# Performance work log

Measured on AMD Instinct MI355X. Metric: run time of the kernel, lower is better.

Reference implementation:

```python
import jax, jax.numpy as jnp
import numpy as np

H_DIM = 64
GRID = 8
NS = 2.0  # neighborhood_size


def _pool_seq(hidden, pos):
    # hidden: (P, H_DIM) hidden states of peds in one scene; pos: (P, 2) end positions
    P = hidden.shape[0]
    g2 = GRID * GRID
    tl_x = pos[:, 0] - NS / 2
    tl_y = pos[:, 1] + NS / 2
    br_x = pos[:, 0] + NS / 2
    br_y = pos[:, 1] - NS / 2
    # pair (i, j): grid of ped i (rows), position of ped j (cols)
    ox = pos[None, :, 0]
    oy = pos[None, :, 1]
    cell_x = jnp.floor((ox - tl_x[:, None]) / NS * GRID)
    cell_y = jnp.floor((tl_y[:, None] - oy) / NS * GRID)
    grid_pos = (cell_x + cell_y * GRID).astype(jnp.int32)
    # out-of-bound if outside neighborhood box OR i == j (diagonal forced out)
    oob = ((ox >= br_x[:, None]) | (ox <= tl_x[:, None])
           | (oy >= tl_y[:, None]) | (oy <= br_y[:, None])
           | jnp.eye(P, dtype=bool))
    idx = grid_pos + 1 + (jnp.arange(P, dtype=jnp.int32) * g2)[:, None]
    idx = jnp.where(oob, 0, idx)  # slot 0 is the trash bin (dropped below)
    src = jnp.broadcast_to(hidden[None], (P, P, H_DIM)).reshape(P * P, H_DIM)
    buf = jnp.zeros((P * g2 + 1, H_DIM), hidden.dtype)
    buf = buf.at[idx.reshape(-1)].add(src)
    return buf[1:].reshape(P, g2 * H_DIM)


def reference(h_states, seq_start_end, end_pos, rel_pos, W, b):
    B = end_pos.shape[0]
    S = seq_start_end.shape[0]
    P = B // S  # equal-length scenes -> static reshape
    hidden = h_states.reshape(-1, H_DIM).reshape(S, P, H_DIM)
    pos = end_pos.reshape(S, P, 2)
    pooled = jax.vmap(_pool_seq)(hidden, pos).reshape(B, GRID * GRID * H_DIM)
    # make_mlp([4096, 1024], relu, batch_norm=False): Linear -> ReLU
    return jax.nn.relu(pooled @ W + b)


def setup_inputs():
    key = jax.random.key(0)
    k0, k1, k2, k3 = jax.random.split(key, 4)
    S, P = 64, 64
    B = S * P
    bottleneck = 1024
    feat = GRID * GRID * H_DIM  # 4096
    h_states = jax.random.normal(k0, (1, B, H_DIM), jnp.float32)
    starts = jnp.arange(S, dtype=jnp.int32) * P
    seq_start_end = jnp.stack([starts, starts + P], axis=1)
    end_pos = jax.random.normal(k1, (B, 2), jnp.float32)
    rel_pos = jax.random.normal(k2, (B, 2), jnp.float32)
    W = jax.random.normal(k3, (feat, bottleneck), jnp.float32) * 0.02
    b = jnp.zeros((bottleneck,), jnp.float32)
    return {"h_states": h_states, "seq_start_end": seq_start_end,
            "end_pos": end_pos, "rel_pos": rel_pos, "W": W, "b": b}
```

## Files before the change

### kernel.cpp

```cpp
#include <hip/hip_runtime.h>


#define BM 128
#define BN 64
#define BK 128

typedef short short8 __attribute__((ext_vector_type(8)));
typedef short short4v __attribute__((ext_vector_type(4)));
typedef float floatx16 __attribute__((ext_vector_type(16)));

__device__ inline short f2bf(float x) {
    union { float f; unsigned u; } v; v.f = x;
    unsigned r = v.u + 0x7fffu + ((v.u >> 16) & 1u);
    return (short)(r >> 16);
}

__device__ inline void gload_lds16(const void* g, void* l) {
    __builtin_amdgcn_global_load_lds(
        (const __attribute__((address_space(1))) void*)g,
        (__attribute__((address_space(3))) void*)l,
        16, 0, 0);
}

__global__ __launch_bounds__(256) void prep_kernel(
    const float* __restrict__ h,
    const float* __restrict__ pos,
    short* __restrict__ pooled,
    const float* __restrict__ W,
    short* __restrict__ Wt,
    int K, int N, int poolBlocks)
{
    __shared__ __align__(16) unsigned char sh[18944];
    const int tid = threadIdx.x;

    if ((int)blockIdx.x < poolBlocks) {
        float* hs = (float*)sh;
        float* px = (float*)(sh + 16384);
        float* py = (float*)(sh + 16640);
        unsigned long long* wmask = (unsigned long long*)(sh + 16896);

        const int lane = tid & 63;
        const int w    = tid >> 6;
        const int s    = blockIdx.x >> 4;
        const int grp  = blockIdx.x & 15;
        const size_t base = (size_t)s * 64;

        const float4* hv  = (const float4*)(h + base * 64);
        float4*       hsv = (float4*)hs;
        #pragma unroll
        for (int c = 0; c < 4; ++c) hsv[tid + c * 256] = hv[tid + c * 256];
        if (tid < 64) {
            float2 p = ((const float2*)pos)[base + tid];
            px[tid] = p.x; py[tid] = p.y;
        }
        wmask[w * 64 + lane] = 0ull;
        __syncthreads();

        const int i = grp * 4 + w;
        const float tlx = px[i] - 1.0f;
        const float tly = py[i] + 1.0f;
        const float brx = px[i] + 1.0f;
        const float bry = py[i] - 1.0f;

        {
            const int j = lane;
            const float ox = px[j], oy = py[j];
            if (ox < brx && ox > tlx && oy < tly && oy > bry && j != i) {
                int cx = (int)floorf((ox - tlx) * 4.0f);
                int cy = (int)floorf((tly - oy) * 4.0f);
                atomicOr(&wmask[w * 64 + cx + cy * 8], 1ull << j);
            }
        }

        const int d = lane;
        const size_t orow = (base + i) * 4096;
        for (int c = 0; c < 64; ++c) {
            unsigned long long m = wmask[w * 64 + c];
            float a0 = 0.f, a1 = 0.f;
            while (m) {
                int j0 = __builtin_ctzll(m); m &= m - 1;
                if (m) {
                    int j1 = __builtin_ctzll(m); m &= m - 1;
                    a1 += hs[j1 * 64 + d];
                }
                a0 += hs[j0 * 64 + d];
            }
            pooled[orow + c * 64 + d] = f2bf(a0 + a1);
        }
    } else {
        float* t = (float*)sh;
        const int bid = blockIdx.x - poolBlocks;
        const int k0 = (bid & 63) * 64;
        const int n0 = (bid >> 6) * 64;

        const int r  = tid >> 4;
        const int cq = (tid & 15) * 4;
        #pragma unroll
        for (int i2 = 0; i2 < 4; ++i2) {
            const int row = r + i2 * 16;
            float4 v = *(const float4*)&W[(size_t)(k0 + row) * N + n0 + cq];
            t[row * 65 + cq + 0] = v.x; t[row * 65 + cq + 1] = v.y;
            t[row * 65 + cq + 2] = v.z; t[row * 65 + cq + 3] = v.w;
        }
        __syncthreads();
        const int nl = tid >> 4;
        const int kq = (tid & 15) * 4;
        #pragma unroll
        for (int i2 = 0; i2 < 4; ++i2) {
            const int n = nl + i2 * 16;
            short4v o;
            o.x = f2bf(t[(kq + 0) * 65 + n]); o.y = f2bf(t[(kq + 1) * 65 + n]);
            o.z = f2bf(t[(kq + 2) * 65 + n]); o.w = f2bf(t[(kq + 3) * 65 + n]);
            *(short4v*)&Wt[(size_t)(n0 + n) * K + k0 + kq] = o;
        }
    }
}

__global__ __launch_bounds__(256) void gemm_bias_relu(
    const short* __restrict__ A,
    const short* __restrict__ Bt,
    const float* __restrict__ bias,
    float* __restrict__ out,
    int M, int N, int K)
{
    __shared__ __align__(16) short As[BM * BK];
    __shared__ __align__(16) short Bs[BN * BK];

    const int tid  = threadIdx.x;
    const int lane = tid & 63;
    const int wave = tid >> 6;
    const int wr = wave >> 1;
    const int wc = wave & 1;
    const int nl = lane & 31;
    const int hl = lane >> 5;
    const int ml = lane & 15;

    const int b  = blockIdx.x;
    const int ib = b >> 3;
    const int m0 = ((b & 7) * 4 + (ib >> 4)) * BM;
    const int n0 = (ib & 15) * BN;

    const int r4   = lane >> 4;
    const int slot = lane & 15;

    const short* ag[8];
    const short* bg[4];
    #pragma unroll
    for (int c = 0; c < 8; ++c) {
        const int gi = c * 4 + wave;
        const int rl = gi * 4 + r4;
        ag[c] = A + (size_t)(m0 + rl) * K + (slot ^ (rl & 15)) * 8;
    }
    #pragma unroll
    for (int c = 0; c < 4; ++c) {
        const int gi = c * 4 + wave;
        const int rl = gi * 4 + r4;
        bg[c] = Bt + (size_t)(n0 + rl) * K + (slot ^ (rl & 15)) * 8;
    }

    floatx16 acc[2];
    #pragma unroll
    for (int mt = 0; mt < 2; ++mt)
        #pragma unroll
        for (int r = 0; r < 16; ++r) acc[mt][r] = 0.f;

    for (int kb = 0; kb < K; kb += BK) {
        if (kb) __syncthreads();
        #pragma unroll
        for (int c = 0; c < 8; ++c) {
            gload_lds16(ag[c], &As[(c * 4 + wave) * 512]);
            ag[c] += BK;
        }
        #pragma unroll
        for (int c = 0; c < 4; ++c) {
            gload_lds16(bg[c], &Bs[(c * 4 + wave) * 512]);
            bg[c] += BK;
        }
        __syncthreads();

        #pragma unroll
        for (int t = 0; t < 8; ++t) {
            const int g  = 2 * t + hl;
            short8 a0 = *(const short8*)&As[(wr * 64 +      nl) * BK + ((g ^ ml) * 8)];
            short8 a1 = *(const short8*)&As[(wr * 64 + 32 + nl) * BK + ((g ^ ml) * 8)];
            short8 bfr = *(const short8*)&Bs[(wc * 32 +     nl) * BK + ((g ^ ml) * 8)];
            acc[0] = __builtin_amdgcn_mfma_f32_32x32x16_bf16(a0, bfr, acc[0], 0, 0, 0);
            acc[1] = __builtin_amdgcn_mfma_f32_32x32x16_bf16(a1, bfr, acc[1], 0, 0, 0);
        }
    }

    const int gn = n0 + wc * 32 + nl;
    const float bv = bias[gn];
    #pragma unroll
    for (int mt = 0; mt < 2; ++mt) {
        #pragma unroll
        for (int r = 0; r < 16; ++r) {
            const int row32 = (r & 3) + 8 * (r >> 2) + 4 * hl;
            const int gm = m0 + wr * 64 + mt * 32 + row32;
            float v = acc[mt][r] + bv;
            out[(size_t)gm * N + gn] = v > 0.f ? v : 0.f;
        }
    }
}

extern "C" void kernel_launch(void* const* d_in, const int* in_sizes, int n_in,
                              void* d_out, int out_size, void* d_ws, size_t ws_size,
                              hipStream_t stream) {
    const float* h    = (const float*)d_in[0];
    const float* pos  = (const float*)d_in[2];
    const float* W    = (const float*)d_in[4];
    const float* bias = (const float*)d_in[5];

    const int B = in_sizes[0] / 64;
    const int N = in_sizes[5];
    const int K = 64 * 64;

    short* pooled = (short*)d_ws;
    short* Wt     = pooled + (size_t)B * K;
    float* out    = (float*)d_out;

    const int poolBlocks = B / 4;
    const int castBlocks = (K / 64) * (N / 64);
    prep_kernel<<<poolBlocks + castBlocks, 256, 0, stream>>>(
        h, pos, pooled, W, Wt, K, N, poolBlocks);
    gemm_bias_relu<<<(B / BM) * (N / BN), 256, 0, stream>>>(
        pooled, Wt, bias, out, B, N, K);
}
```

Before: 133.3 us.

## Double-buffer GEMM LDS tiles and enlarge N tile to 128

The bf16 GEMM now uses a 128x128 output tile with BK=64, so each wave computes a 2x2 set of 32x32 MFMA tiles and reuses each loaded fragment more often. LDS is double-buffered: the next K slice is fetched with global_load_lds while the current one is consumed, leaving one barrier per iteration. This is meant to hide global-load latency and raise arithmetic intensity. The cost is half as many blocks (256 workgroups), more accumulator registers, and a changed XOR swizzle for the 64-wide rows.

```diff
diff --git a/kernel.cpp b/kernel.cpp
--- a/kernel.cpp
+++ b/kernel.cpp
@@ -2,8 +2,8 @@
 
 
 #define BM 128
-#define BN 64
-#define BK 128
+#define BN 128
+#define BK 64
 
 typedef short short8 __attribute__((ext_vector_type(8)));
 typedef short short4v __attribute__((ext_vector_type(4)));
@@ -123,8 +123,7 @@
     float* __restrict__ out,
     int M, int N, int K)
 {
-    __shared__ __align__(16) short As[BM * BK];
-    __shared__ __align__(16) short Bs[BN * BK];
+    __shared__ __align__(16) short smem[2][2][BM * BK];
 
     const int tid  = threadIdx.x;
     const int lane = tid & 63;
@@ -133,72 +132,81 @@
     const int wc = wave & 1;
     const int nl = lane & 31;
     const int hl = lane >> 5;
-    const int ml = lane & 15;
+    const int k7 = nl & 7;
 
     const int b  = blockIdx.x;
     const int ib = b >> 3;
-    const int m0 = ((b & 7) * 4 + (ib >> 4)) * BM;
-    const int n0 = (ib & 15) * BN;
-
-    const int r4   = lane >> 4;
-    const int slot = lane & 15;
-
-    const short* ag[8];
+    const int m0 = ((b & 7) * 4 + (ib >> 3)) * BM;
+    const int n0 = (ib & 7) * BN;
+
+    const int r8    = lane >> 3;
+    const int slot3 = lane & 7;
+
+    const short* ag[4];
     const short* bg[4];
     #pragma unroll
-    for (int c = 0; c < 8; ++c) {
-        const int gi = c * 4 + wave;
-        const int rl = gi * 4 + r4;
-        ag[c] = A + (size_t)(m0 + rl) * K + (slot ^ (rl & 15)) * 8;
-    }
-    #pragma unroll
     for (int c = 0; c < 4; ++c) {
-        const int gi = c * 4 + wave;
-        const int rl = gi * 4 + r4;
-        bg[c] = Bt + (size_t)(n0 + rl) * K + (slot ^ (rl & 15)) * 8;
-    }
-
-    floatx16 acc[2];
-    #pragma unroll
-    for (int mt = 0; mt < 2; ++mt)
-        #pragma unroll
-        for (int r = 0; r < 16; ++r) acc[mt][r] = 0.f;
+        const int g  = c * 4 + wave;
+        const int rl = g * 8 + r8;
+        ag[c] = A  + (size_t)(m0 + rl) * K + (slot3 ^ (rl & 7)) * 8;
+        bg[c] = Bt + (size_t)(n0 + rl) * K + (slot3 ^ (rl & 7)) * 8;
+    }
+
+    floatx16 acc[2][2];
+    #pragma unroll
+    for (int i = 0; i < 2; ++i)
+        #pragma unroll
+        for (int j = 0; j < 2; ++j)
+            #pragma unroll
+            for (int r = 0; r < 16; ++r) acc[i][j][r] = 0.f;
+
+    #pragma unroll
+    for (int c = 0; c < 4; ++c) {
+        gload_lds16(ag[c], &smem[0][0][(c * 4 + wave) * 512]);
+        gload_lds16(bg[c], &smem[0][1][(c * 4 + wave) * 512]);
+        ag[c] += BK; bg[c] += BK;
+    }
+    __syncthreads();
 
     for (int kb = 0; kb < K; kb += BK) {
-        if (kb) __syncthreads();
-        #pragma unroll
-        for (int c = 0; c < 8; ++c) {
-            gload_lds16(ag[c], &As[(c * 4 + wave) * 512]);
-            ag[c] += BK;
-        }
-        #pragma unroll
-        for (int c = 0; c < 4; ++c) {
-            gload_lds16(bg[c], &Bs[(c * 4 + wave) * 512]);
-            bg[c] += BK;
+        const int bu = (kb >> 6) & 1;
+        if (kb + BK < K) {
+            #pragma unroll
+            for (int c = 0; c < 4; ++c) {
+                gload_lds16(ag[c], &smem[bu ^ 1][0][(c * 4 + wave) * 512]);
+                gload_lds16(bg[c], &smem[bu ^ 1][1][(c * 4 + wave) * 512]);
+                ag[c] += BK; bg[c] += BK;
+            }
+        }
+        #pragma unroll
+        for (int t = 0; t < 4; ++t) {
+            const int g = 2 * t + hl;
+            const int go = (g ^ k7) * 8;
+            short8 a0 = *(const short8*)&smem[bu][0][(wr * 64 +      nl) * BK + go];
+            short8 a1 = *(const short8*)&smem[bu][0][(wr * 64 + 32 + nl) * BK + go];
+            short8 b0 = *(const short8*)&smem[bu][1][(wc * 64 +      nl) * BK + go];
+            short8 b1 = *(const short8*)&smem[bu][1][(wc * 64 + 32 + nl) * BK + go];
+            acc[0][0] = __builtin_amdgcn_mfma_f32_32x32x16_bf16(a0, b0, acc[0][0], 0, 0, 0);
+            acc[0][1] = __builtin_amdgcn_mfma_f32_32x32x16_bf16(a0, b1, acc[0][1], 0, 0, 0);
+            acc[1][0] = __builtin_amdgcn_mfma_f32_32x32x16_bf16(a1, b0, acc[1][0], 0, 0, 0);
+            acc[1][1] = __builtin_amdgcn_mfma_f32_32x32x16_bf16(a1, b1, acc[1][1], 0, 0, 0);
         }
         __syncthreads();
-
-        #pragma unroll
-        for (int t = 0; t < 8; ++t) {
-            const int g  = 2 * t + hl;
-            short8 a0 = *(const short8*)&As[(wr * 64 +      nl) * BK + ((g ^ ml) * 8)];
-            short8 a1 = *(const short8*)&As[(wr * 64 + 32 + nl) * BK + ((g ^ ml) * 8)];
-            short8 bfr = *(const short8*)&Bs[(wc * 32 +     nl) * BK + ((g ^ ml) * 8)];
-            acc[0] = __builtin_amdgcn_mfma_f32_32x32x16_bf16(a0, bfr, acc[0], 0, 0, 0);
-            acc[1] = __builtin_amdgcn_mfma_f32_32x32x16_bf16(a1, bfr, acc[1], 0, 0, 0);
-        }
-    }
-
-    const int gn = n0 + wc * 32 + nl;
-    const float bv = bias[gn];
-    #pragma unroll
-    for (int mt = 0; mt < 2; ++mt) {
-        #pragma unroll
-        for (int r = 0; r < 16; ++r) {
-            const int row32 = (r & 3) + 8 * (r >> 2) + 4 * hl;
-            const int gm = m0 + wr * 64 + mt * 32 + row32;
-            float v = acc[mt][r] + bv;
-            out[(size_t)gm * N + gn] = v > 0.f ? v : 0.f;
+    }
+
+    #pragma unroll
+    for (int jt = 0; jt < 2; ++jt) {
+        const int gn = n0 + wc * 64 + jt * 32 + nl;
+        const float bv = bias[gn];
+        #pragma unroll
+        for (int mt = 0; mt < 2; ++mt) {
+            #pragma unroll
+            for (int r = 0; r < 16; ++r) {
+                const int row32 = (r & 3) + 8 * (r >> 2) + 4 * hl;
+                const int gm = m0 + wr * 64 + mt * 32 + row32;
+                float v = acc[mt][jt][r] + bv;
+                out[(size_t)gm * N + gn] = v > 0.f ? v : 0.f;
+            }
         }
     }
 }
```

Measured after the change: 135.6 us. Within noise of the previous version (+1.8%).

## Write pooled A in MFMA fragment layout and load A directly from global

Applied to the files above, without the earlier changes.

The pooling stage now writes the bf16 pooled matrix in a pre-swizzled layout that matches the 32x32x16 MFMA operand fragment. The GEMM then reads A fragments straight from global memory into registers and drops the A staging through LDS. This removes LDS traffic, LDS capacity and global_load_lds work for A, which could allow higher occupancy. In exchange, A loads are no longer shared across the two column waves, so global/L2 reads of A double, and the pooling stores become scattered with a stride.

```diff
diff --git a/kernel.cpp b/kernel.cpp
--- a/kernel.cpp
+++ b/kernel.cpp
@@ -25,7 +25,7 @@
 __global__ __launch_bounds__(256) void prep_kernel(
     const float* __restrict__ h,
     const float* __restrict__ pos,
-    short* __restrict__ pooled,
+    short* __restrict__ Afr,
     const float* __restrict__ W,
     short* __restrict__ Wt,
     int K, int N, int poolBlocks)
@@ -73,19 +73,24 @@
         }
 
         const int d = lane;
-        const size_t orow = (base + i) * 4096;
+        const int m = (int)base + i;
+        const size_t pbase = (size_t)(m >> 5) * 131072
+                           + (size_t)(d >> 4) * 512
+                           + (size_t)((d >> 3) & 1) * 256
+                           + (size_t)(m & 31) * 8
+                           + (size_t)(d & 7);
         for (int c = 0; c < 64; ++c) {
-            unsigned long long m = wmask[w * 64 + c];
+            unsigned long long mk = wmask[w * 64 + c];
             float a0 = 0.f, a1 = 0.f;
-            while (m) {
-                int j0 = __builtin_ctzll(m); m &= m - 1;
-                if (m) {
-                    int j1 = __builtin_ctzll(m); m &= m - 1;
+            while (mk) {
+                int j0 = __builtin_ctzll(mk); mk &= mk - 1;
+                if (mk) {
+                    int j1 = __builtin_ctzll(mk); mk &= mk - 1;
                     a1 += hs[j1 * 64 + d];
                 }
                 a0 += hs[j0 * 64 + d];
             }
-            pooled[orow + c * 64 + d] = f2bf(a0 + a1);
+            Afr[pbase + (size_t)c * 2048] = f2bf(a0 + a1);
         }
     } else {
         float* t = (float*)sh;
@@ -117,13 +122,12 @@
 }
 
 __global__ __launch_bounds__(256) void gemm_bias_relu(
-    const short* __restrict__ A,
+    const short* __restrict__ Afr,
     const short* __restrict__ Bt,
     const float* __restrict__ bias,
     float* __restrict__ out,
     int M, int N, int K)
 {
-    __shared__ __align__(16) short As[BM * BK];
     __shared__ __align__(16) short Bs[BN * BK];
 
     const int tid  = threadIdx.x;
@@ -137,20 +141,12 @@
 
     const int b  = blockIdx.x;
     const int ib = b >> 3;
-    const int m0 = ((b & 7) * 4 + (ib >> 4)) * BM;
+    const int mb = (b & 7) * 4 + (ib >> 4);
     const int n0 = (ib & 15) * BN;
 
     const int r4   = lane >> 4;
     const int slot = lane & 15;
-
-    const short* ag[8];
     const short* bg[4];
-    #pragma unroll
-    for (int c = 0; c < 8; ++c) {
-        const int gi = c * 4 + wave;
-        const int rl = gi * 4 + r4;
-        ag[c] = A + (size_t)(m0 + rl) * K + (slot ^ (rl & 15)) * 8;
-    }
     #pragma unroll
     for (int c = 0; c < 4; ++c) {
         const int gi = c * 4 + wave;
@@ -158,6 +154,9 @@
         bg[c] = Bt + (size_t)(n0 + rl) * K + (slot ^ (rl & 15)) * 8;
     }
 
+    const short* a0p = Afr + ((size_t)(mb * 4 + wr * 2) * 256) * 512 + (size_t)lane * 8;
+    const short* a1p = a0p + 131072;
+
     floatx16 acc[2];
     #pragma unroll
     for (int mt = 0; mt < 2; ++mt)
@@ -167,23 +166,20 @@
     for (int kb = 0; kb < K; kb += BK) {
         if (kb) __syncthreads();
         #pragma unroll
-        for (int c = 0; c < 8; ++c) {
-            gload_lds16(ag[c], &As[(c * 4 + wave) * 512]);
-            ag[c] += BK;
-        }
-        #pragma unroll
         for (int c = 0; c < 4; ++c) {
             gload_lds16(bg[c], &Bs[(c * 4 + wave) * 512]);
             bg[c] += BK;
         }
         __syncthreads();
 
+        const int tbase = kb >> 4;
         #pragma unroll
         for (int t = 0; t < 8; ++t) {
-            const int g  = 2 * t + hl;
-            short8 a0 = *(const short8*)&As[(wr * 64 +      nl) * BK + ((g ^ ml) * 8)];
-            short8 a1 = *(const short8*)&As[(wr * 64 + 32 + nl) * BK + ((g ^ ml) * 8)];
-            short8 bfr = *(const short8*)&Bs[(wc * 32 +     nl) * BK + ((g ^ ml) * 8)];
+            const int koff = (tbase + t) * 512;
+            short8 a0 = *(const short8*)(a0p + koff);
+            short8 a1 = *(const short8*)(a1p + koff);
+            const int g = 2 * t + hl;
+            short8 bfr = *(const short8*)&Bs[(wc * 32 + nl) * BK + ((g ^ ml) * 8)];
             acc[0] = __builtin_amdgcn_mfma_f32_32x32x16_bf16(a0, bfr, acc[0], 0, 0, 0);
             acc[1] = __builtin_amdgcn_mfma_f32_32x32x16_bf16(a1, bfr, acc[1], 0, 0, 0);
         }
@@ -196,7 +192,7 @@
         #pragma unroll
         for (int r = 0; r < 16; ++r) {
             const int row32 = (r & 3) + 8 * (r >> 2) + 4 * hl;
-            const int gm = m0 + wr * 64 + mt * 32 + row32;
+            const int gm = mb * BM + wr * 64 + mt * 32 + row32;
             float v = acc[mt][r] + bv;
             out[(size_t)gm * N + gn] = v > 0.f ? v : 0.f;
         }
@@ -215,14 +211,14 @@
     const int N = in_sizes[5];
     const int K = 64 * 64;
 
-    short* pooled = (short*)d_ws;
-    short* Wt     = pooled + (size_t)B * K;
-    float* out    = (float*)d_out;
+    short* Afr = (short*)d_ws;
+    short* Wt  = Afr + (size_t)B * K;
+    float* out = (float*)d_out;
 
     const int poolBlocks = B / 4;
     const int castBlocks = (K / 64) * (N / 64);
     prep_kernel<<<poolBlocks + castBlocks, 256, 0, stream>>>(
-        h, pos, pooled, W, Wt, K, N, poolBlocks);
+        h, pos, Afr, W, Wt, K, N, poolBlocks);
     gemm_bias_relu<<<(B / BM) * (N / BN), 256, 0, stream>>>(
-        pooled, Wt, bias, out, B, N, K);
-}
+        Afr, Wt, bias, out, B, N, K);
+}
```

Result: slower. 178.9 us (+34.3%).

## Reshape GEMM tile to 64x128 with two waves each computing 64x64

Applied to the files above, without the earlier changes.

Switches the GEMM block tile from 128x64 with four waves to 64x128 with two waves. Each wave now computes a 2x2 grid of 32x32 MFMA tiles, reusing its A and B fragments across four MFMAs per LDS read. The block-to-tile mapping is adjusted for the new grid shape. The aim is a higher MFMA-to-LDS-read ratio per wave, at the cost of fewer threads per block to issue the global-to-LDS loads and possibly lower occupancy from the larger accumulator.

```diff
diff --git a/kernel.cpp b/kernel.cpp
--- a/kernel.cpp
+++ b/kernel.cpp
@@ -1,8 +1,8 @@
 #include <hip/hip_runtime.h>
 
 
-#define BM 128
-#define BN 64
+#define BM 64
+#define BN 128
 #define BK 128
 
 typedef short short8 __attribute__((ext_vector_type(8)));
@@ -116,7 +116,7 @@
     }
 }
 
-__global__ __launch_bounds__(256) void gemm_bias_relu(
+__global__ __launch_bounds__(128) void gemm_bias_relu(
     const short* __restrict__ A,
     const short* __restrict__ Bt,
     const float* __restrict__ bias,
@@ -129,51 +129,52 @@
     const int tid  = threadIdx.x;
     const int lane = tid & 63;
     const int wave = tid >> 6;
-    const int wr = wave >> 1;
-    const int wc = wave & 1;
     const int nl = lane & 31;
     const int hl = lane >> 5;
     const int ml = lane & 15;
 
     const int b  = blockIdx.x;
     const int ib = b >> 3;
-    const int m0 = ((b & 7) * 4 + (ib >> 4)) * BM;
-    const int n0 = (ib & 15) * BN;
+    const int mb = (b & 7) * 8 + (ib >> 3);
+    const int m0 = mb * BM;
+    const int n0 = (ib & 7) * BN;
 
     const int r4   = lane >> 4;
     const int slot = lane & 15;
 
     const short* ag[8];
-    const short* bg[4];
+    const short* bg[16];
     #pragma unroll
     for (int c = 0; c < 8; ++c) {
-        const int gi = c * 4 + wave;
+        const int gi = c * 2 + wave;
         const int rl = gi * 4 + r4;
         ag[c] = A + (size_t)(m0 + rl) * K + (slot ^ (rl & 15)) * 8;
     }
     #pragma unroll
-    for (int c = 0; c < 4; ++c) {
-        const int gi = c * 4 + wave;
+    for (int c = 0; c < 16; ++c) {
+        const int gi = c * 2 + wave;
         const int rl = gi * 4 + r4;
         bg[c] = Bt + (size_t)(n0 + rl) * K + (slot ^ (rl & 15)) * 8;
     }
 
-    floatx16 acc[2];
-    #pragma unroll
-    for (int mt = 0; mt < 2; ++mt)
-        #pragma unroll
-        for (int r = 0; r < 16; ++r) acc[mt][r] = 0.f;
+    floatx16 acc[2][2];
+    #pragma unroll
+    for (int i = 0; i < 2; ++i)
+        #pragma unroll
+        for (int j = 0; j < 2; ++j)
+            #pragma unroll
+            for (int r = 0; r < 16; ++r) acc[i][j][r] = 0.f;
 
     for (int kb = 0; kb < K; kb += BK) {
         if (kb) __syncthreads();
         #pragma unroll
         for (int c = 0; c < 8; ++c) {
-            gload_lds16(ag[c], &As[(c * 4 + wave) * 512]);
+            gload_lds16(ag[c], &As[(c * 2 + wave) * 512]);
             ag[c] += BK;
         }
         #pragma unroll
-        for (int c = 0; c < 4; ++c) {
-            gload_lds16(bg[c], &Bs[(c * 4 + wave) * 512]);
+        for (int c = 0; c < 16; ++c) {
+            gload_lds16(bg[c], &Bs[(c * 2 + wave) * 512]);
             bg[c] += BK;
         }
         __syncthreads();
@@ -181,24 +182,31 @@
         #pragma unroll
         for (int t = 0; t < 8; ++t) {
             const int g  = 2 * t + hl;
-            short8 a0 = *(const short8*)&As[(wr * 64 +      nl) * BK + ((g ^ ml) * 8)];
-            short8 a1 = *(const short8*)&As[(wr * 64 + 32 + nl) * BK + ((g ^ ml) * 8)];
-            short8 bfr = *(const short8*)&Bs[(wc * 32 +     nl) * BK + ((g ^ ml) * 8)];
-            acc[0] = __builtin_amdgcn_mfma_f32_32x32x16_bf16(a0, bfr, acc[0], 0, 0, 0);
-            acc[1] = __builtin_amdgcn_mfma_f32_32x32x16_bf16(a1, bfr, acc[1], 0, 0, 0);
-        }
-    }
-
-    const int gn = n0 + wc * 32 + nl;
-    const float bv = bias[gn];
-    #pragma unroll
-    for (int mt = 0; mt < 2; ++mt) {
-        #pragma unroll
-        for (int r = 0; r < 16; ++r) {
-            const int row32 = (r & 3) + 8 * (r >> 2) + 4 * hl;
-            const int gm = m0 + wr * 64 + mt * 32 + row32;
-            float v = acc[mt][r] + bv;
-            out[(size_t)gm * N + gn] = v > 0.f ? v : 0.f;
+            const int go = (g ^ ml) * 8;
+            short8 a0 = *(const short8*)&As[(nl)      * BK + go];
+            short8 a1 = *(const short8*)&As[(32 + nl) * BK + go];
+            short8 b0 = *(const short8*)&Bs[(wave * 64 +      nl) * BK + go];
+            short8 b1 = *(const short8*)&Bs[(wave * 64 + 32 + nl) * BK + go];
+            acc[0][0] = __builtin_amdgcn_mfma_f32_32x32x16_bf16(a0, b0, acc[0][0], 0, 0, 0);
+            acc[0][1] = __builtin_amdgcn_mfma_f32_32x32x16_bf16(a0, b1, acc[0][1], 0, 0, 0);
+            acc[1][0] = __builtin_amdgcn_mfma_f32_32x32x16_bf16(a1, b0, acc[1][0], 0, 0, 0);
+            acc[1][1] = __builtin_amdgcn_mfma_f32_32x32x16_bf16(a1, b1, acc[1][1], 0, 0, 0);
+        }
+    }
+
+    #pragma unroll
+    for (int jt = 0; jt < 2; ++jt) {
+        const int gn = n0 + wave * 64 + jt * 32 + nl;
+        const float bv = bias[gn];
+        #pragma unroll
+        for (int mt = 0; mt < 2; ++mt) {
+            #pragma unroll
+            for (int r = 0; r < 16; ++r) {
+                const int row32 = (r & 3) + 8 * (r >> 2) + 4 * hl;
+                const int gm = m0 + mt * 32 + row32;
+                float v = acc[mt][jt][r] + bv;
+                out[(size_t)gm * N + gn] = v > 0.f ? v : 0.f;
+            }
         }
     }
 }
@@ -223,6 +231,6 @@
     const int castBlocks = (K / 64) * (N / 64);
     prep_kernel<<<poolBlocks + castBlocks, 256, 0, stream>>>(
         h, pos, pooled, W, Wt, K, N, poolBlocks);
-    gemm_bias_relu<<<(B / BM) * (N / BN), 256, 0, stream>>>(
+    gemm_bias_relu<<<(B / BM) * (N / BN), 128, 0, stream>>>(
         pooled, Wt, bias, out, B, N, K);
 }
```

Measured after the change: 145.8 us. 1.09x slower.
